# Performance work log

Measured on AMD Instinct MI355X. Metric: run time of the kernel, lower is better.

## Reference

```python
import jax, jax.numpy as jnp
from jax import lax
import numpy as np

B, S, D, H = 256, 2048, 16, 128
HH = H // 2  # head hidden = 64


def _p(key, shape, scale=0.05):
    return scale * jax.random.normal(key, shape, dtype=jnp.float32)


def setup_inputs() -> dict:
    key = jax.random.key(0)
    ks = jax.random.split(key, 12)
    return {
        "x": jax.random.normal(ks[0], (B, S, D), dtype=jnp.float32),
        # LSTM layer 0 (PyTorch gate order: i, f, g, o along the 4H axis)
        "W_ih0": _p(ks[1], (4 * H, D)),
        "W_hh0": _p(ks[2], (4 * H, H)),
        "b_ih0": jnp.zeros((4 * H,), jnp.float32),
        "b_hh0": jnp.zeros((4 * H,), jnp.float32),
        # LSTM layer 1
        "W_ih1": _p(ks[3], (4 * H, H)),
        "W_hh1": _p(ks[4], (4 * H, H)),
        "b_ih1": jnp.zeros((4 * H,), jnp.float32),
        "b_hh1": jnp.zeros((4 * H,), jnp.float32),
        # return head: Linear(H, H//2) -> LeakyReLU -> Linear(H//2, 1)
        "Wr1": _p(ks[5], (HH, H)), "br1": jnp.zeros((HH,), jnp.float32),
        "Wr2": _p(ks[6], (1, HH)), "br2": jnp.zeros((1,), jnp.float32),
        # vol head: Linear -> LeakyReLU -> Linear -> Softplus
        "Wv1": _p(ks[7], (HH, H)), "bv1": jnp.zeros((HH,), jnp.float32),
        "Wv2": _p(ks[8], (1, HH)), "bv2": jnp.zeros((1,), jnp.float32),
    }


def _lstm_layer(x, W_ih, W_hh, b_ih, b_hh):
    # x: (B, S, Din) -> hs: (B, S, H); PyTorch gate order i, f, g, o
    b, s, _ = x.shape
    h_dim = W_hh.shape[1]
    xg = jnp.einsum('bsd,gd->bsg', x, W_ih) + (b_ih + b_hh)  # (B, S, 4H)

    def step(carry, xg_t):
        h, c = carry
        g = xg_t + h @ W_hh.T
        i, f, gc, o = jnp.split(g, 4, axis=-1)
        i = jax.nn.sigmoid(i)
        f = jax.nn.sigmoid(f)
        gc = jnp.tanh(gc)
        o = jax.nn.sigmoid(o)
        c = f * c + i * gc
        h = o * jnp.tanh(c)
        return (h, c), h

    h0 = jnp.zeros((b, h_dim), x.dtype)
    (hN, cN), hs = lax.scan(step, (h0, jnp.zeros_like(h0)), jnp.swapaxes(xg, 0, 1))
    return jnp.swapaxes(hs, 0, 1), hN, cN


def reference(x, W_ih0, W_hh0, b_ih0, b_hh0, W_ih1, W_hh1, b_ih1, b_hh1,
              Wr1, br1, Wr2, br2, Wv1, bv1, Wv2, bv2):
    h1, hN0, cN0 = _lstm_layer(x, W_ih0, W_hh0, b_ih0, b_hh0)
    # inter-layer dropout is inactive at inference (eval mode)
    h2, hN1, cN1 = _lstm_layer(h1, W_ih1, W_hh1, b_ih1, b_hh1)
    # return head
    r = jax.nn.leaky_relu(jnp.einsum('bsh,kh->bsk', h2, Wr1) + br1)
    returns = jnp.einsum('bsk,ok->bso', r, Wr2) + br2
    # volatility head
    v = jax.nn.leaky_relu(jnp.einsum('bsh,kh->bsk', h2, Wv1) + bv1)
    volatility = jax.nn.softplus(jnp.einsum('bsk,ok->bso', v, Wv2) + bv2)
    hidden_h = jnp.stack([hN0, hN1], axis=0)  # (num_layers, B, H)
    hidden_c = jnp.stack([cN0, cN1], axis=0)
    return returns, volatility, hidden_h, hidden_c
```

## Files before the change

### kernel.cpp

```cpp
#include <hip/hip_runtime.h>
#include <hip/hip_bf16.h>

#define B_ 256
#define S_ 2048
#define D_ 16
#define H_ 128

typedef unsigned int u32;
typedef unsigned short u16;
typedef _Float16 h2t __attribute__((ext_vector_type(2)));

#define RET0 ((size_t)0)
#define VOL0 ((size_t)524288)
#define HH0  ((size_t)1048576)
#define HC0  ((size_t)1114112)

__device__ __forceinline__ float fdot2(u32 a, u32 b, float c) {
    return __builtin_amdgcn_fdot2(__builtin_bit_cast(h2t, a),
                                  __builtin_bit_cast(h2t, b), c, false);
}
__device__ __forceinline__ u32 packh2(float a, float b) {
    h2t h; h[0] = (_Float16)a; h[1] = (_Float16)b;
    return __builtin_bit_cast(u32, h);
}
__device__ __forceinline__ float sigm(float x) {
    return __builtin_amdgcn_rcpf(1.f + __builtin_amdgcn_exp2f(-1.44269504f * x));
}
__device__ __forceinline__ float tanh_(float x) {
    return 2.f * __builtin_amdgcn_rcpf(1.f + __builtin_amdgcn_exp2f(-2.88539008f * x)) - 1.f;
}
__device__ __forceinline__ float softplus_(float x) {
    if (x > 20.f) return x;
    const float e = __builtin_amdgcn_exp2f(1.44269504f * x);
    return 0.69314718f * __builtin_amdgcn_logf(1.f + e);
}
__device__ __forceinline__ float dnb1(float a) {
    return __builtin_bit_cast(float, __builtin_amdgcn_update_dpp(
        0, __builtin_bit_cast(int, a), 0xB1, 0xF, 0xF, true));
}

__global__
__attribute__((amdgpu_waves_per_eu(4, 4)))
__launch_bounds__(1024) void k_l0(
    const float* __restrict__ x, const float* __restrict__ Wih,
    const float* __restrict__ Whh, const float* __restrict__ bih,
    const float* __restrict__ bhh, u32* __restrict__ h1out,
    float* __restrict__ out)
{
    __shared__ u32 xp2[2][2048];
    __shared__ float gates[8][128][4];
    __shared__ u32 hb[2][64];
    __shared__ u32 och[2048];

    const int tid = threadIdx.x, b = blockIdx.x;
    const int ksl = tid >> 7, m = tid & 127;

    u32 wx[4], wh[32];
#pragma unroll
    for (int g = 0; g < 4; ++g) {
        const int row = g * H_ + m;
        const float2 f2 = *(const float2*)(Wih + row * D_ + ksl * 2);
        wx[g] = packh2(f2.x, f2.y);
        const float4* whr = (const float4*)(Whh + row * H_ + ksl * 16);
#pragma unroll
        for (int j = 0; j < 4; ++j) {
            const float4 f = whr[j];
            wh[g * 8 + 2 * j]     = packh2(f.x, f.y);
            wh[g * 8 + 2 * j + 1] = packh2(f.z, f.w);
        }
    }
    float bias[4], c = 0.f;
    if (tid < 128) {
#pragma unroll
        for (int g = 0; g < 4; ++g) bias[g] = bih[g * H_ + tid] + bhh[g * H_ + tid];
    }

    const float* xb = x + (size_t)b * S_ * D_;
    {
        const float4 v = *(const float4*)(xb + tid * 4);
        xp2[0][2 * tid] = packh2(v.x, v.y);
        xp2[0][2 * tid + 1] = packh2(v.z, v.w);
    }
    if (tid < 128) ((u32*)hb)[tid] = 0u;
    __syncthreads();

    for (int t = 0; t < S_; ++t) {
        if ((t & 255) == 0 && t < S_ - 256) {
            const int nw = (t >> 8) + 1;
            const float4 v = *(const float4*)(xb + (size_t)nw * 4096 + tid * 4);
            xp2[nw & 1][2 * tid] = packh2(v.x, v.y);
            xp2[nw & 1][2 * tid + 1] = packh2(v.z, v.w);
        }
        const u32 xv = xp2[(t >> 8) & 1][(t & 255) * 8 + ksl];
        const u32* hs = &hb[(t + 1) & 1][ksl * 8];
        const uint4 h0 = *(const uint4*)(hs);
        const uint4 h1v = *(const uint4*)(hs + 4);
        float a0 = fdot2(xv, wx[0], 0.f), a1 = fdot2(xv, wx[1], 0.f);
        float a2 = fdot2(xv, wx[2], 0.f), a3 = fdot2(xv, wx[3], 0.f);
#define L0G(comp, j)                                                           \
        a0 = fdot2(comp, wh[j], a0);        a1 = fdot2(comp, wh[8 + (j)], a1); \
        a2 = fdot2(comp, wh[16 + (j)], a2); a3 = fdot2(comp, wh[24 + (j)], a3);
        L0G(h0.x, 0) L0G(h0.y, 1) L0G(h0.z, 2) L0G(h0.w, 3)
        L0G(h1v.x, 4) L0G(h1v.y, 5) L0G(h1v.z, 6) L0G(h1v.w, 7)
#undef L0G
        float4 part; part.x = a0; part.y = a1; part.z = a2; part.w = a3;
        *(float4*)&gates[ksl][m][0] = part;
        __syncthreads();
        if (tid < 128) {
            float4 s = *(const float4*)&gates[0][tid][0];
#pragma unroll
            for (int k = 1; k < 8; ++k) {
                const float4 p = *(const float4*)&gates[k][tid][0];
                s.x += p.x; s.y += p.y; s.z += p.z; s.w += p.w;
            }
            const float ig = sigm(s.x + bias[0]);
            const float fg = sigm(s.y + bias[1]);
            const float gc = tanh_(s.z + bias[2]);
            const float og = sigm(s.w + bias[3]);
            c = fg * c + ig * gc;
            const float hv = og * tanh_(c);
            const u32 pp = packh2(hv, dnb1(hv));
            if (!(tid & 1)) {
                hb[t & 1][tid >> 1] = pp;
                och[(t & 31) * 64 + (tid >> 1)] = pp;
            }
            if (t == S_ - 1) {
                out[HH0 + (size_t)b * H_ + tid] = hv;
                out[HC0 + (size_t)b * H_ + tid] = c;
            }
        }
        __syncthreads();
        if ((t & 31) == 31) {
            if (tid < 512) {
                u32* dst = h1out + ((size_t)b * S_ + (t - 31)) * 64;
                *(uint4*)(dst + tid * 4) = *(const uint4*)(&och[tid * 4]);
            }
            __syncthreads();
        }
    }
}

__global__
__attribute__((amdgpu_waves_per_eu(4, 4)))
__launch_bounds__(1024) void k_l1(
    u32* __restrict__ hws,
    const float* __restrict__ Wih, const float* __restrict__ Whh,
    const float* __restrict__ bih, const float* __restrict__ bhh,
    float* __restrict__ out)
{
    __shared__ u32 h1w[64 * 80];
    __shared__ float gates[8][128][4];
    __shared__ u32 hp[2][80];
    __shared__ u32 och[2048];

    const int tid = threadIdx.x, b = blockIdx.x;
    const int ksl = tid >> 7, m = tid & 127;

    u32 w[64];
    const float* Wsel = (ksl < 4) ? Wih : Whh;
    const int colb = (ksl & 3) * 32;
#pragma unroll
    for (int g = 0; g < 4; ++g) {
        const int row = g * H_ + m;
        const float4* wr_ = (const float4*)(Wsel + row * H_ + colb);
#pragma unroll
        for (int j = 0; j < 8; ++j) {
            const float4 f = wr_[j];
            w[g * 16 + 2 * j]     = packh2(f.x, f.y);
            w[g * 16 + 2 * j + 1] = packh2(f.z, f.w);
        }
    }
    float bias[4], c = 0.f;
    if (tid < 128) {
#pragma unroll
        for (int g = 0; g < 4; ++g) bias[g] = bih[g * H_ + tid] + bhh[g * H_ + tid];
    }
    if (tid < 160) ((u32*)hp)[tid] = 0u;
    __syncthreads();

    u32* hbase = hws + (size_t)b * S_ * 64;
    for (int u = 0; u < S_; ++u) {
        if ((u & 63) == 0) {
            const uint4 v = *(const uint4*)(hbase + (size_t)u * 64 + tid * 4);
            const int st = tid >> 4, p4 = tid & 15;
            *(uint4*)(&h1w[st * 80 + (p4 >> 2) * 20 + (p4 & 3) * 4]) = v;
            __syncthreads();
        }
        const u32* sel = (ksl < 4) ? &h1w[(u & 63) * 80 + ksl * 20]
                                   : &hp[(u + 1) & 1][(ksl - 4) * 20];
        float a0 = 0.f, a1 = 0.f, a2 = 0.f, a3 = 0.f;
#pragma unroll
        for (int p = 0; p < 4; ++p) {
            const uint4 v = *(const uint4*)(sel + p * 4);
            a0 = fdot2(v.x, w[4 * p], a0);      a0 = fdot2(v.y, w[4 * p + 1], a0);
            a0 = fdot2(v.z, w[4 * p + 2], a0);  a0 = fdot2(v.w, w[4 * p + 3], a0);
            a1 = fdot2(v.x, w[16 + 4 * p], a1); a1 = fdot2(v.y, w[17 + 4 * p], a1);
            a1 = fdot2(v.z, w[18 + 4 * p], a1); a1 = fdot2(v.w, w[19 + 4 * p], a1);
            a2 = fdot2(v.x, w[32 + 4 * p], a2); a2 = fdot2(v.y, w[33 + 4 * p], a2);
            a2 = fdot2(v.z, w[34 + 4 * p], a2); a2 = fdot2(v.w, w[35 + 4 * p], a2);
            a3 = fdot2(v.x, w[48 + 4 * p], a3); a3 = fdot2(v.y, w[49 + 4 * p], a3);
            a3 = fdot2(v.z, w[50 + 4 * p], a3); a3 = fdot2(v.w, w[51 + 4 * p], a3);
        }
        float4 part; part.x = a0; part.y = a1; part.z = a2; part.w = a3;
        *(float4*)&gates[ksl][m][0] = part;
        __syncthreads();
        if (tid < 128) {
            float4 s = *(const float4*)&gates[0][tid][0];
#pragma unroll
            for (int k = 1; k < 8; ++k) {
                const float4 p = *(const float4*)&gates[k][tid][0];
                s.x += p.x; s.y += p.y; s.z += p.z; s.w += p.w;
            }
            const float ig = sigm(s.x + bias[0]);
            const float fg = sigm(s.y + bias[1]);
            const float gc = tanh_(s.z + bias[2]);
            const float og = sigm(s.w + bias[3]);
            c = fg * c + ig * gc;
            const float hv = og * tanh_(c);
            const u32 pp = packh2(hv, dnb1(hv));
            if (!(tid & 1)) {
                const int p2 = tid >> 1;
                hp[u & 1][(p2 >> 4) * 20 + (p2 & 15)] = pp;
                och[(u & 31) * 64 + p2] = pp;
            }
            if (u == S_ - 1) {
                out[HH0 + 32768 + (size_t)b * H_ + tid] = hv;
                out[HC0 + 32768 + (size_t)b * H_ + tid] = c;
            }
        }
        __syncthreads();
        if ((u & 31) == 31) {
            if (tid < 512) {
                u32* dst = hbase + (size_t)(u - 31) * 64;
                *(uint4*)(dst + tid * 4) = *(const uint4*)(&och[tid * 4]);
            }
            __syncthreads();
        }
    }
}

__global__ __launch_bounds__(256) void k_heads(
    const u32* __restrict__ h2p,
    const float* __restrict__ Wr1, const float* __restrict__ br1,
    const float* __restrict__ Wr2, const float* __restrict__ br2,
    const float* __restrict__ Wv1, const float* __restrict__ bv1,
    const float* __restrict__ Wv2, const float* __restrict__ bv2,
    float* __restrict__ out)
{
    __shared__ u32 wr[64 * 64], wv[64 * 64];
    __shared__ float w2r[64], w2v[64], b1r[64], b1v[64];

    const int tid = threadIdx.x;
    for (int i = tid; i < 4096; i += 256) {
        wr[i] = packh2(Wr1[2 * i], Wr1[2 * i + 1]);
        wv[i] = packh2(Wv1[2 * i], Wv1[2 * i + 1]);
    }
    if (tid < 64) {
        w2r[tid] = Wr2[tid]; w2v[tid] = Wv2[tid];
        b1r[tid] = br1[tid]; b1v[tid] = bv1[tid];
    }
    __syncthreads();

    const size_t bs = (size_t)blockIdx.x * 256 + tid;
    u32 hq[64];
    const u32* src = h2p + bs * 64;
#pragma unroll
    for (int j4 = 0; j4 < 16; ++j4) {
        const uint4 v = *(const uint4*)(src + j4 * 4);
        hq[j4 * 4] = v.x; hq[j4 * 4 + 1] = v.y; hq[j4 * 4 + 2] = v.z; hq[j4 * 4 + 3] = v.w;
    }
    float ret = br2[0], vol = bv2[0];
    for (int k = 0; k < 64; ++k) {
        float r = b1r[k], v = b1v[k];
#pragma unroll
        for (int j = 0; j < 64; ++j) r = fdot2(hq[j], wr[k * 64 + j], r);
#pragma unroll
        for (int j = 0; j < 64; ++j) v = fdot2(hq[j], wv[k * 64 + j], v);
        r = r > 0.f ? r : 0.01f * r;
        v = v > 0.f ? v : 0.01f * v;
        ret += r * w2r[k];
        vol += v * w2v[k];
    }
    out[RET0 + bs] = ret;
    out[VOL0 + bs] = softplus_(vol);
}

extern "C" void kernel_launch(void* const* d_in, const int* in_sizes, int n_in,
                              void* d_out, int out_size, void* d_ws, size_t ws_size,
                              hipStream_t stream) {
    (void)in_sizes; (void)n_in; (void)out_size; (void)ws_size;
    const float* x    = (const float*)d_in[0];
    const float* Wih0 = (const float*)d_in[1];
    const float* Whh0 = (const float*)d_in[2];
    const float* bih0 = (const float*)d_in[3];
    const float* bhh0 = (const float*)d_in[4];
    const float* Wih1 = (const float*)d_in[5];
    const float* Whh1 = (const float*)d_in[6];
    const float* bih1 = (const float*)d_in[7];
    const float* bhh1 = (const float*)d_in[8];
    const float* Wr1  = (const float*)d_in[9];
    const float* br1  = (const float*)d_in[10];
    const float* Wr2  = (const float*)d_in[11];
    const float* br2  = (const float*)d_in[12];
    const float* Wv1  = (const float*)d_in[13];
    const float* bv1  = (const float*)d_in[14];
    const float* Wv2  = (const float*)d_in[15];
    const float* bv2  = (const float*)d_in[16];
    u32* hws  = (u32*)d_ws;
    float* out = (float*)d_out;

    k_l0<<<B_, 1024, 0, stream>>>(x, Wih0, Whh0, bih0, bhh0, hws, out);
    k_l1<<<B_, 1024, 0, stream>>>(hws, Wih1, Whh1, bih1, bhh1, out);
    k_heads<<<2048, 256, 0, stream>>>(hws, Wr1, br1, Wr2, br2,
                                      Wv1, bv1, Wv2, bv2, out);
}
```

Measured before the change: 3.554 ms.

## Restructure LSTM layer-0 to 512 threads with redundant per-wave gate reduction

Layer-0 kernel moves from 1024 to 512 threads, each holding twice as many recurrent weights (4-way K split instead of 8). Every wave now redundantly reduces the gate partials and computes the cell update for its own 32 units, writing h into a per-wave buffer. That cuts the per-step barriers from two to one, using a double-buffered gates array. The h1 output staging is also double-buffered so global writes happen without extra barriers. The cost is duplicated activation math, more registers per thread, and a longer dot-product chain per thread.

```diff
diff --git a/kernel.cpp b/kernel.cpp
--- a/kernel.cpp
+++ b/kernel.cpp
@@ -7,7 +7,6 @@
 #define H_ 128
 
 typedef unsigned int u32;
-typedef unsigned short u16;
 typedef _Float16 h2t __attribute__((ext_vector_type(2)));
 
 #define RET0 ((size_t)0)
@@ -39,104 +38,111 @@
         0, __builtin_bit_cast(int, a), 0xB1, 0xF, 0xF, true));
 }
 
-__global__
-__attribute__((amdgpu_waves_per_eu(4, 4)))
-__launch_bounds__(1024) void k_l0(
+__global__ __launch_bounds__(512, 2) void k_l0(
     const float* __restrict__ x, const float* __restrict__ Wih,
     const float* __restrict__ Whh, const float* __restrict__ bih,
     const float* __restrict__ bhh, u32* __restrict__ h1out,
     float* __restrict__ out)
 {
     __shared__ u32 xp2[2][2048];
-    __shared__ float gates[8][128][4];
-    __shared__ u32 hb[2][64];
-    __shared__ u32 och[2048];
+    __shared__ float gates[2][4][128][4];
+    __shared__ u32 hb[8][16];
+    __shared__ u32 och[2][2048];
 
     const int tid = threadIdx.x, b = blockIdx.x;
     const int ksl = tid >> 7, m = tid & 127;
-
-    u32 wx[4], wh[32];
+    const int wv = tid >> 6, j = tid & 63;
+    const int unit = (ksl << 5) + (j & 31);
+
+    u32 wx[8], wh[64];
 #pragma unroll
     for (int g = 0; g < 4; ++g) {
         const int row = g * H_ + m;
-        const float2 f2 = *(const float2*)(Wih + row * D_ + ksl * 2);
-        wx[g] = packh2(f2.x, f2.y);
-        const float4* whr = (const float4*)(Whh + row * H_ + ksl * 16);
-#pragma unroll
-        for (int j = 0; j < 4; ++j) {
-            const float4 f = whr[j];
-            wh[g * 8 + 2 * j]     = packh2(f.x, f.y);
-            wh[g * 8 + 2 * j + 1] = packh2(f.z, f.w);
-        }
-    }
-    float bias[4], c = 0.f;
-    if (tid < 128) {
-#pragma unroll
-        for (int g = 0; g < 4; ++g) bias[g] = bih[g * H_ + tid] + bhh[g * H_ + tid];
-    }
+        const float4 fx = *(const float4*)(Wih + row * D_ + ksl * 4);
+        wx[g * 2]     = packh2(fx.x, fx.y);
+        wx[g * 2 + 1] = packh2(fx.z, fx.w);
+        const float4* whr = (const float4*)(Whh + row * H_ + ksl * 32);
+#pragma unroll
+        for (int q = 0; q < 8; ++q) {
+            const float4 f = whr[q];
+            wh[g * 16 + 2 * q]     = packh2(f.x, f.y);
+            wh[g * 16 + 2 * q + 1] = packh2(f.z, f.w);
+        }
+    }
+    const float bias0 = bih[unit] + bhh[unit];
+    const float bias1 = bih[128 + unit] + bhh[128 + unit];
+    const float bias2 = bih[256 + unit] + bhh[256 + unit];
+    const float bias3 = bih[384 + unit] + bhh[384 + unit];
 
     const float* xb = x + (size_t)b * S_ * D_;
-    {
-        const float4 v = *(const float4*)(xb + tid * 4);
-        xp2[0][2 * tid] = packh2(v.x, v.y);
-        xp2[0][2 * tid + 1] = packh2(v.z, v.w);
+#pragma unroll
+    for (int k = 0; k < 2; ++k) {
+        const int i = tid + k * 512;
+        const float4 v = *(const float4*)(xb + i * 4);
+        xp2[0][2 * i]     = packh2(v.x, v.y);
+        xp2[0][2 * i + 1] = packh2(v.z, v.w);
     }
     if (tid < 128) ((u32*)hb)[tid] = 0u;
+    float c = 0.f;
     __syncthreads();
 
     for (int t = 0; t < S_; ++t) {
         if ((t & 255) == 0 && t < S_ - 256) {
             const int nw = (t >> 8) + 1;
-            const float4 v = *(const float4*)(xb + (size_t)nw * 4096 + tid * 4);
-            xp2[nw & 1][2 * tid] = packh2(v.x, v.y);
-            xp2[nw & 1][2 * tid + 1] = packh2(v.z, v.w);
-        }
-        const u32 xv = xp2[(t >> 8) & 1][(t & 255) * 8 + ksl];
-        const u32* hs = &hb[(t + 1) & 1][ksl * 8];
-        const uint4 h0 = *(const uint4*)(hs);
-        const uint4 h1v = *(const uint4*)(hs + 4);
-        float a0 = fdot2(xv, wx[0], 0.f), a1 = fdot2(xv, wx[1], 0.f);
-        float a2 = fdot2(xv, wx[2], 0.f), a3 = fdot2(xv, wx[3], 0.f);
-#define L0G(comp, j)                                                           \
-        a0 = fdot2(comp, wh[j], a0);        a1 = fdot2(comp, wh[8 + (j)], a1); \
-        a2 = fdot2(comp, wh[16 + (j)], a2); a3 = fdot2(comp, wh[24 + (j)], a3);
-        L0G(h0.x, 0) L0G(h0.y, 1) L0G(h0.z, 2) L0G(h0.w, 3)
-        L0G(h1v.x, 4) L0G(h1v.y, 5) L0G(h1v.z, 6) L0G(h1v.w, 7)
-#undef L0G
+#pragma unroll
+            for (int k = 0; k < 2; ++k) {
+                const int i = tid + k * 512;
+                const float4 v = *(const float4*)(xb + (size_t)nw * 4096 + i * 4);
+                xp2[nw & 1][2 * i]     = packh2(v.x, v.y);
+                xp2[nw & 1][2 * i + 1] = packh2(v.z, v.w);
+            }
+        }
+        const uint2 xv = *(const uint2*)&xp2[(t >> 8) & 1][(t & 255) * 8 + ksl * 2];
+        const uint4* hq = (const uint4*)hb[wv];
+        const uint4 h0 = hq[0], h1 = hq[1], h2 = hq[2], h3 = hq[3];
+        float a0 = fdot2(xv.x, wx[0], 0.f); a0 = fdot2(xv.y, wx[1], a0);
+        float a1 = fdot2(xv.x, wx[2], 0.f); a1 = fdot2(xv.y, wx[3], a1);
+        float a2 = fdot2(xv.x, wx[4], 0.f); a2 = fdot2(xv.y, wx[5], a2);
+        float a3 = fdot2(xv.x, wx[6], 0.f); a3 = fdot2(xv.y, wx[7], a3);
+#define DG(vv, p)                                                              \
+        a0 = fdot2(vv, wh[p], a0);        a1 = fdot2(vv, wh[16 + (p)], a1);    \
+        a2 = fdot2(vv, wh[32 + (p)], a2); a3 = fdot2(vv, wh[48 + (p)], a3);
+        DG(h0.x, 0) DG(h0.y, 1) DG(h0.z, 2) DG(h0.w, 3)
+        DG(h1.x, 4) DG(h1.y, 5) DG(h1.z, 6) DG(h1.w, 7)
+        DG(h2.x, 8) DG(h2.y, 9) DG(h2.z, 10) DG(h2.w, 11)
+        DG(h3.x, 12) DG(h3.y, 13) DG(h3.z, 14) DG(h3.w, 15)
+#undef DG
         float4 part; part.x = a0; part.y = a1; part.z = a2; part.w = a3;
-        *(float4*)&gates[ksl][m][0] = part;
+        *(float4*)&gates[t & 1][ksl][m][0] = part;
         __syncthreads();
-        if (tid < 128) {
-            float4 s = *(const float4*)&gates[0][tid][0];
-#pragma unroll
-            for (int k = 1; k < 8; ++k) {
-                const float4 p = *(const float4*)&gates[k][tid][0];
-                s.x += p.x; s.y += p.y; s.z += p.z; s.w += p.w;
-            }
-            const float ig = sigm(s.x + bias[0]);
-            const float fg = sigm(s.y + bias[1]);
-            const float gc = tanh_(s.z + bias[2]);
-            const float og = sigm(s.w + bias[3]);
-            c = fg * c + ig * gc;
-            const float hv = og * tanh_(c);
-            const u32 pp = packh2(hv, dnb1(hv));
-            if (!(tid & 1)) {
-                hb[t & 1][tid >> 1] = pp;
-                och[(t & 31) * 64 + (tid >> 1)] = pp;
-            }
-            if (t == S_ - 1) {
-                out[HH0 + (size_t)b * H_ + tid] = hv;
-                out[HC0 + (size_t)b * H_ + tid] = c;
-            }
-        }
-        __syncthreads();
-        if ((t & 31) == 31) {
-            if (tid < 512) {
-                u32* dst = h1out + ((size_t)b * S_ + (t - 31)) * 64;
-                *(uint4*)(dst + tid * 4) = *(const uint4*)(&och[tid * 4]);
-            }
-            __syncthreads();
-        }
+        if ((t & 31) == 0 && t) {
+            u32* dst = h1out + ((size_t)b * S_ + (t - 32)) * 64;
+            *(uint4*)(dst + tid * 4) = *(const uint4*)&och[((t >> 5) & 1) ^ 1][tid * 4];
+        }
+        const float4 s0 = *(const float4*)&gates[t & 1][0][unit][0];
+        const float4 s1 = *(const float4*)&gates[t & 1][1][unit][0];
+        const float4 s2 = *(const float4*)&gates[t & 1][2][unit][0];
+        const float4 s3 = *(const float4*)&gates[t & 1][3][unit][0];
+        const float ig = sigm((s0.x + s1.x) + (s2.x + s3.x) + bias0);
+        const float fg = sigm((s0.y + s1.y) + (s2.y + s3.y) + bias1);
+        const float gc = tanh_((s0.z + s1.z) + (s2.z + s3.z) + bias2);
+        const float og = sigm((s0.w + s1.w) + (s2.w + s3.w) + bias3);
+        c = fg * c + ig * gc;
+        const float h = og * tanh_(c);
+        const u32 pp = packh2(h, dnb1(h));
+        if ((j & 33) == 0) {
+            hb[wv][j >> 1] = pp;
+            if (!(wv & 1)) och[(t >> 5) & 1][(t & 31) * 64 + (unit >> 1)] = pp;
+        }
+        if (t == S_ - 1 && !(wv & 1) && j < 32) {
+            out[HH0 + (size_t)b * H_ + unit] = h;
+            out[HC0 + (size_t)b * H_ + unit] = c;
+        }
+    }
+    __syncthreads();
+    {
+        u32* dst = h1out + ((size_t)b * S_ + (S_ - 32)) * 64;
+        *(uint4*)(dst + tid * 4) = *(const uint4*)&och[1][tid * 4];
     }
 }
 
@@ -164,10 +170,10 @@
         const int row = g * H_ + m;
         const float4* wr_ = (const float4*)(Wsel + row * H_ + colb);
 #pragma unroll
-        for (int j = 0; j < 8; ++j) {
-            const float4 f = wr_[j];
-            w[g * 16 + 2 * j]     = packh2(f.x, f.y);
-            w[g * 16 + 2 * j + 1] = packh2(f.z, f.w);
+        for (int q = 0; q < 8; ++q) {
+            const float4 f = wr_[q];
+            w[g * 16 + 2 * q]     = packh2(f.x, f.y);
+            w[g * 16 + 2 * q + 1] = packh2(f.z, f.w);
         }
     }
     float bias[4], c = 0.f;
@@ -267,7 +273,8 @@
 #pragma unroll
     for (int j4 = 0; j4 < 16; ++j4) {
         const uint4 v = *(const uint4*)(src + j4 * 4);
-        hq[j4 * 4] = v.x; hq[j4 * 4 + 1] = v.y; hq[j4 * 4 + 2] = v.z; hq[j4 * 4 + 3] = v.w;
+        hq[j4 * 4] = v.x; hq[j4 * 4 + 1] = v.y;
+        hq[j4 * 4 + 2] = v.z; hq[j4 * 4 + 3] = v.w;
     }
     float ret = br2[0], vol = bv2[0];
     for (int k = 0; k < 64; ++k) {
@@ -309,7 +316,7 @@
     u32* hws  = (u32*)d_ws;
     float* out = (float*)d_out;
 
-    k_l0<<<B_, 1024, 0, stream>>>(x, Wih0, Whh0, bih0, bhh0, hws, out);
+    k_l0<<<B_, 512, 0, stream>>>(x, Wih0, Whh0, bih0, bhh0, hws, out);
     k_l1<<<B_, 1024, 0, stream>>>(hws, Wih1, Whh1, bih1, bhh1, out);
     k_heads<<<2048, 256, 0, stream>>>(hws, Wr1, br1, Wr2, br2,
                                       Wv1, bv1, Wv2, bv2, out);
```

New measurement: 3.361 ms. 5.4% less time.
